# Kernel optimization log

Hardware: AMD Instinct MI355X
Metric: run time of the kernel (lower is better)

## Reference

```python
import jax, jax.numpy as jnp
import numpy as np

NUM_TRAIN = 256  # num_train_anchors
N, A, T = 8, 131072, 64


def _make_boxes(key, shape2):
    # shape2 = (..., 2) of (y, x); returns valid boxes (y1, x1, y2, x2) in [0, 1]
    k1, k2 = jax.random.split(key)
    c1 = jax.random.uniform(k1, shape2, dtype=jnp.float32)
    c2 = jax.random.uniform(k2, shape2, dtype=jnp.float32)
    lo = jnp.minimum(c1, c2)
    hi = jnp.maximum(c1, c2)
    return jnp.stack([lo[..., 0], lo[..., 1], hi[..., 0], hi[..., 1]], axis=-1)


def setup_inputs() -> dict:
    key = jax.random.key(0)
    ka, kt, kp, kn = jax.random.split(key, 4)
    return {
        "anchors": _make_boxes(ka, (N, A, 2)),
        "true_bboxes": _make_boxes(kt, (N, T, 2)),
        "rand_pos": jax.random.uniform(kp, (N, A), dtype=jnp.float32),
        "rand_neg": jax.random.uniform(kn, (N, A), dtype=jnp.float32),
    }


def _bbox_overlap(anchors, gt):
    # anchors [A,4], gt [T,4] -> IoU [A,T]
    ay1, ax1, ay2, ax2 = [anchors[:, i] for i in range(4)]
    gy1, gx1, gy2, gx2 = [gt[:, i] for i in range(4)]
    a_area = (ay2 - ay1) * (ax2 - ax1)                       # [A]
    g_area = (gy2 - gy1) * (gx2 - gx1)                       # [T]
    ih = jnp.clip(jnp.minimum(ay2[:, None], gy2[None, :]) - jnp.maximum(ay1[:, None], gy1[None, :]), 0.0)
    iw = jnp.clip(jnp.minimum(ax2[:, None], gx2[None, :]) - jnp.maximum(ax1[:, None], gx1[None, :]), 0.0)
    inter = ih * iw                                          # [A,T]
    union = a_area[:, None] + g_area[None, :] - inter
    return jnp.where(union > 0, inter / jnp.where(union > 0, union, 1.0), 0.0)


def _rank_of(scores):
    # rank[i] = position of element i in ascending sort of scores
    order = jnp.argsort(scores)
    return jnp.zeros(scores.shape[0], jnp.int32).at[order].set(jnp.arange(scores.shape[0], dtype=jnp.int32))


def _compute_bbox_deltas(anchors, gt):
    # standard (dy, dx, dh, dw) encoding with safe denominators
    ah = anchors[:, 2] - anchors[:, 0]
    aw = anchors[:, 3] - anchors[:, 1]
    acy = anchors[:, 0] + 0.5 * ah
    acx = anchors[:, 1] + 0.5 * aw
    gh = gt[:, 2] - gt[:, 0]
    gw = gt[:, 3] - gt[:, 1]
    gcy = gt[:, 0] + 0.5 * gh
    gcx = gt[:, 1] + 0.5 * gw
    ah_s = jnp.where(ah > 0, ah, 1.0)
    aw_s = jnp.where(aw > 0, aw, 1.0)
    gh_s = jnp.where(gh > 0, gh, 1.0)
    gw_s = jnp.where(gw > 0, gw, 1.0)
    return jnp.stack([(gcy - acy) / ah_s, (gcx - acx) / aw_s,
                      jnp.log(gh_s / ah_s), jnp.log(gw_s / aw_s)], axis=-1)


def _get_targets(anchors, gt, r_pos, r_neg):
    na = anchors.shape[0]
    # strip_out_of_bounds_anchors: zero out anchors falling outside [0,1]^2 (keeps static shape)
    inb = (anchors[:, 0] >= 0) & (anchors[:, 1] >= 0) & (anchors[:, 2] <= 1) & (anchors[:, 3] <= 1)
    anchors = jnp.where(inb[:, None], anchors, 0.0)

    overlaps = _bbox_overlap(anchors, gt)                    # [A,T]

    # --- class assignment ---
    iou_max_val = jnp.max(overlaps, axis=1)                  # [A]
    classes = jnp.full((na,), -1, jnp.int32)
    classes = jnp.where(iou_max_val < 0.3, 0, classes)
    iou_max_anchor = jnp.argmax(overlaps, axis=0)            # [T] best anchor per gt
    pos_anchor = jnp.zeros((na,), jnp.int32).at[iou_max_anchor].set(1)
    classes = jnp.where(pos_anchor > 0, 1, classes)
    classes = jnp.where(iou_max_val >= 0.7, 1, classes)

    # --- subsample positives to NUM_TRAIN//2 (uniform random subset) ---
    pos = classes > 0
    rank_p = _rank_of(jnp.where(pos, r_pos, jnp.inf))
    keep_pos = pos & (rank_p < NUM_TRAIN // 2)
    classes = jnp.where(pos & ~keep_pos, -1, classes)
    n_pos = jnp.sum(keep_pos.astype(jnp.int32))

    # --- subsample negatives to NUM_TRAIN - n_pos ---
    desired_neg = NUM_TRAIN - n_pos
    neg = classes == 0
    rank_n = _rank_of(jnp.where(neg, r_neg, jnp.inf))
    keep_neg = neg & (rank_n < desired_neg)
    classes = jnp.where(neg & ~keep_neg, -1, classes)

    # --- deltas for positive anchors ---
    best_gt = jnp.argmax(overlaps, axis=1)                   # [A]
    deltas = _compute_bbox_deltas(anchors, gt[best_gt])      # [A,4]
    deltas = jnp.where((classes > 0)[:, None], deltas, 0.0)
    return classes, deltas


def reference(anchors, true_bboxes, rand_pos, rand_neg):
    classes, deltas = jax.vmap(_get_targets)(anchors, true_bboxes, rand_pos, rand_neg)
    return classes, deltas
```

## Files before the change

kernel.cpp:

```cpp
#include <hip/hip_runtime.h>
#include <stdint.h>

#define N_B 8
#define A_N 131072
#define T_N 64
#define NUM_TRAIN 256
#define NEG_TAU 0.05f
#define ITEM_CAP 512
#define HSET 512
#define APT 2
#define SEG_A 512
#define GBLK_A 256
#define CAPP 128
#define BLK_C 128
#define SEG_C 1024

typedef unsigned long long u64;
typedef unsigned int u32;

__device__ __forceinline__ float iou_one(float ay1, float ax1, float ay2, float ax2,
                                         float a_area, float gy1, float gx1, float gy2,
                                         float gx2, float g_area) {
#pragma clang fp contract(off)
    float ih = fmaxf(fminf(ay2, gy2) - fmaxf(ay1, gy1), 0.0f);
    float iw = fmaxf(fminf(ax2, gx2) - fmaxf(ax1, gx1), 0.0f);
    float inter = ih * iw;
    float uni = (a_area + g_area) - inter;
    return uni > 0.0f ? inter / uni : 0.0f;
}

__global__ void __launch_bounds__(256) k_main(const float4* __restrict__ anchors4,
                                              const float4* __restrict__ gts4,
                                              const float* __restrict__ rpos,
                                              const float* __restrict__ rneg,
                                              unsigned char* __restrict__ preclass,
                                              long long* __restrict__ colpack,
                                              u64* __restrict__ pos_list,
                                              u64* __restrict__ neg_list,
                                              int* __restrict__ bcp, int* __restrict__ bcn) {
    __shared__ float4 gbox[T_N];
    __shared__ float gars[T_N];
    __shared__ u64 cmax[T_N];
    __shared__ int lcnt[2];
    int n = blockIdx.y, bx = blockIdx.x, tid = threadIdx.x, lane = tid & 63;
    int a0 = bx * SEG_A + tid;
    size_t nA = (size_t)n * A_N;

    if (tid < T_N) {
        float4 gb = gts4[n * T_N + tid];
        gbox[tid] = gb;
        {
#pragma clang fp contract(off)
            gars[tid] = (gb.z - gb.x) * (gb.w - gb.y);
        }
        cmax[tid] = 0;
    }
    if (tid < 2) lcnt[tid] = 0;
    __syncthreads();

    float ay1[APT], ax1[APT], ay2[APT], ax2[APT], aar[APT], vmax[APT];
#pragma unroll
    for (int k = 0; k < APT; k++) {
        float4 ab = anchors4[nA + a0 + k * 256];
        float y1 = ab.x, x1 = ab.y, y2 = ab.z, x2 = ab.w;
        bool inb = (y1 >= 0.f) && (x1 >= 0.f) && (y2 <= 1.f) && (x2 <= 1.f);
        if (!inb) { y1 = x1 = y2 = x2 = 0.f; }
        ay1[k] = y1; ax1[k] = x1; ay2[k] = y2; ax2[k] = x2;
        {
#pragma clang fp contract(off)
            aar[k] = (y2 - y1) * (x2 - x1);
        }
        vmax[k] = 0.f;
    }

#pragma unroll 4
    for (int jj = 0; jj < T_N; jj++) {
        int j = (lane + jj) & (T_N - 1);
        float4 gb = gbox[j];
        float gar = gars[j];
        float vb = iou_one(ay1[0], ax1[0], ay2[0], ax2[0], aar[0], gb.x, gb.y, gb.z, gb.w, gar);
        vmax[0] = fmaxf(vmax[0], vb);
        int kb = 0;
#pragma unroll
        for (int k = 1; k < APT; k++) {
            float v = iou_one(ay1[k], ax1[k], ay2[k], ax2[k], aar[k], gb.x, gb.y, gb.z, gb.w, gar);
            vmax[k] = fmaxf(vmax[k], v);
            if (v > vb) { vb = v; kb = k; }
        }
        u64 pk = ((u64)__float_as_uint(vb) << 32) | (u32)(~(u32)(a0 + (kb << 8)));
        atomicMax(&cmax[j], pk);
    }

    size_t segbase = ((size_t)(n * GBLK_A + bx)) << 7;
#pragma unroll
    for (int k = 0; k < APT; k++) {
        int a = a0 + k * 256;
        float vm = vmax[k];
        int c0 = (vm < 0.3f) ? 0 : ((vm >= 0.7f) ? 1 : -1);
        preclass[nA + a] = (unsigned char)(signed char)c0;
        if (c0 == 1) {
            int sl = atomicAdd(&lcnt[0], 1);
            if (sl < CAPP)
                pos_list[segbase + sl] = ((u64)__float_as_uint(rpos[nA + a]) << 32) | (u32)a;
        } else if (c0 == 0) {
            float r = rneg[nA + a];
            if (r < NEG_TAU) {
                int sl = atomicAdd(&lcnt[1], 1);
                if (sl < CAPP)
                    neg_list[segbase + sl] = ((u64)__float_as_uint(r) << 32) | (u32)a;
            }
        }
    }
    __syncthreads();
    if (tid < T_N) atomicMax(&colpack[(n << 6) + tid], (long long)cmax[tid]);
    if (tid == 0) {
        bcp[n * GBLK_A + bx] = lcnt[0] < CAPP ? lcnt[0] : CAPP;
        bcn[n * GBLK_A + bx] = lcnt[1] < CAPP ? lcnt[1] : CAPP;
    }
}

__device__ __forceinline__ bool in_hset(const int* hset, int a) {
    u32 h = ((u32)a * 2654435761u) >> 23 & (HSET - 1);
    while (true) {
        int v = hset[h];
        if (v == -1) return false;
        if (v == a) return true;
        h = (h + 1) & (HSET - 1);
    }
}

__device__ u64 select_kth2(const u64* lists, const int* scnt,
                           const u64* extras, int ecnt, const int* hset, bool use_excl,
                           int k, float scale, u64 ovf_all,
                           int* hist, u64* items, int* misc, int* wsum, u64* result) {
    int tid = threadIdx.x, lane = tid & 63, wid = tid >> 6;
    hist[tid] = 0;
    if (tid == 0) { misc[0] = 0; *result = ovf_all; }
    __syncthreads();

    int c = scnt[tid];
    const ulonglong2* b2 = (const ulonglong2*)(lists + ((size_t)tid << 7));
    int nch = (c + 1) >> 1;

    {
        ulonglong2 q;
        if (nch > 0) q = b2[0];
        for (int ci = 0; ci < nch; ci++) {
            ulonglong2 qn;
            if (ci + 1 < nch) qn = b2[ci + 1];
            {
                u64 p = q.x; int a = (int)(u32)p;
                if (!use_excl || !in_hset(hset, a)) {
                    float v = __uint_as_float((u32)(p >> 32));
                    int bb = (int)(v * scale); bb = bb > 255 ? 255 : bb;
                    atomicAdd(&hist[bb], 1);
                }
            }
            if (2 * ci + 1 < c) {
                u64 p = q.y; int a = (int)(u32)p;
                if (!use_excl || !in_hset(hset, a)) {
                    float v = __uint_as_float((u32)(p >> 32));
                    int bb = (int)(v * scale); bb = bb > 255 ? 255 : bb;
                    atomicAdd(&hist[bb], 1);
                }
            }
            q = qn;
        }
    }
    for (int i = tid; i < ecnt; i += 256) {
        float v = __uint_as_float((u32)(extras[i] >> 32));
        int bb = (int)(v * scale); bb = bb > 255 ? 255 : bb;
        atomicAdd(&hist[bb], 1);
    }
    __syncthreads();

    int h = hist[tid], v = h;
#pragma unroll
    for (int d = 1; d < 64; d <<= 1) {
        int t = __shfl_up(v, d, 64);
        if (lane >= d) v += t;
    }
    if (lane == 63) wsum[wid] = v;
    __syncthreads();
    int base = 0;
    for (int w = 0; w < wid; w++) base += wsum[w];
    int total = wsum[0] + wsum[1] + wsum[2] + wsum[3];
    int incl = base + v, exc = incl - h;
    if (k >= exc && k < incl) { misc[1] = tid; misc[2] = exc; }
    __syncthreads();
    if (k >= total) return ovf_all;
    int b = misc[1], before = misc[2];

    {
        ulonglong2 q;
        if (nch > 0) q = b2[0];
        for (int ci = 0; ci < nch; ci++) {
            ulonglong2 qn;
            if (ci + 1 < nch) qn = b2[ci + 1];
            {
                u64 p = q.x; int a = (int)(u32)p;
                if (!use_excl || !in_hset(hset, a)) {
                    float vv = __uint_as_float((u32)(p >> 32));
                    int bn = (int)(vv * scale); bn = bn > 255 ? 255 : bn;
                    if (bn == b) { int ix = atomicAdd(&misc[0], 1); if (ix < ITEM_CAP) items[ix] = p; }
                }
            }
            if (2 * ci + 1 < c) {
                u64 p = q.y; int a = (int)(u32)p;
                if (!use_excl || !in_hset(hset, a)) {
                    float vv = __uint_as_float((u32)(p >> 32));
                    int bn = (int)(vv * scale); bn = bn > 255 ? 255 : bn;
                    if (bn == b) { int ix = atomicAdd(&misc[0], 1); if (ix < ITEM_CAP) items[ix] = p; }
                }
            }
            q = qn;
        }
    }
    for (int i = tid; i < ecnt; i += 256) {
        u64 p = extras[i];
        float vv = __uint_as_float((u32)(p >> 32));
        int bn = (int)(vv * scale); bn = bn > 255 ? 255 : bn;
        if (bn == b) { int ix = atomicAdd(&misc[0], 1); if (ix < ITEM_CAP) items[ix] = p; }
    }
    __syncthreads();
    int m = misc[0]; m = m < ITEM_CAP ? m : ITEM_CAP;
    int target = k - before;
    for (int i = tid; i < m; i += 256) {
        u64 p = items[i];
        int r = 0;
        for (int j = 0; j < m; j++) r += (items[j] < p);
        if (r == target) *result = p;
    }
    __syncthreads();
    u64 res = *result;
    __syncthreads();
    return res;
}

__global__ void __launch_bounds__(256) k_B(const u64* __restrict__ pos_list,
                                           const u64* __restrict__ neg_list,
                                           const int* __restrict__ bcp,
                                           const int* __restrict__ bcn,
                                           const long long* __restrict__ colpack,
                                           const unsigned char* __restrict__ preclass,
                                           const float* __restrict__ rpos,
                                           int* __restrict__ wnr_g,
                                           u64* __restrict__ cutoff) {
    __shared__ int sbp[GBLK_A], sbn[GBLK_A];
    __shared__ int wnrs[T_N];
    __shared__ u64 extras[T_N];
    __shared__ int hist[256];
    __shared__ u64 items[ITEM_CAP];
    __shared__ int hset[HSET];
    __shared__ int misc[4];
    __shared__ int wsum[4];
    __shared__ int shr[10];
    __shared__ u64 result;
    int n = blockIdx.y, role = blockIdx.x, tid = threadIdx.x, lane = tid & 63, wid = tid >> 6;
    size_t nA = (size_t)n * A_N;

    int pv = bcp[n * GBLK_A + tid];
    sbp[tid] = pv;
    sbn[tid] = bcn[n * GBLK_A + tid];
#pragma unroll
    for (int off = 32; off > 0; off >>= 1) pv += __shfl_xor(pv, off, 64);
    if (lane == 0) shr[wid] = pv;

    for (int i = tid; i < HSET; i += 256) hset[i] = -1;
    __syncthreads();

    if (tid < T_N) {
        u64 m = (u64)colpack[(n << 6) + tid];
        int w = (int)(~(u32)(m & 0xFFFFFFFFull));
        wnrs[tid] = w;
        if (role == 0) wnr_g[n * T_N + tid] = w;
        u32 hh = ((u32)w * 2654435761u) >> 23 & (HSET - 1);
        while (true) {
            int old = atomicCAS(&hset[hh], -1, w);
            if (old == -1 || old == w) break;
            hh = (hh + 1) & (HSET - 1);
        }
    }
    __syncthreads();
    if (tid < T_N) {
        int w = wnrs[tid];
        bool dup = false;
        for (int t2 = 0; t2 < tid; t2++) dup |= (wnrs[t2] == w);
        int pc = (int)(signed char)preclass[nA + w];
        bool val = !dup && (pc != 1);
        u64 mask = __ballot(val);
        if (role == 0 && val) {
            int ix = (int)__popcll(mask & ((1ull << lane) - 1));
            extras[ix] = ((u64)__float_as_uint(rpos[nA + w]) << 32) | (u32)w;
        }
        if (tid == 0) shr[8] = (int)__popcll(mask);
    }
    __syncthreads();
    int extra_cnt = shr[8];
    int P = shr[0] + shr[1] + shr[2] + shr[3] + extra_cnt;

    if (role == 0) {
        u64 cpos = ~0ull;
        if (NUM_TRAIN / 2 < P)
            cpos = select_kth2(pos_list + (((size_t)n * GBLK_A) << 7), sbp,
                               extras, extra_cnt, hset, false,
                               NUM_TRAIN / 2, 256.0f, ~0ull,
                               hist, items, misc, wsum, &result);
        if (tid == 0) cutoff[2 * n] = cpos;
    } else {
        int n_pos = P < NUM_TRAIN / 2 ? P : NUM_TRAIN / 2;
        int k_neg = NUM_TRAIN - n_pos;
        u64 cneg = select_kth2(neg_list + (((size_t)n * GBLK_A) << 7), sbn,
                               nullptr, 0, hset, true,
                               k_neg, 256.0f / NEG_TAU, ((u64)__float_as_uint(NEG_TAU) << 32),
                               hist, items, misc, wsum, &result);
        if (tid == 0) cutoff[2 * n + 1] = cneg;
    }
}

__global__ void __launch_bounds__(256) k_C(const float4* __restrict__ anchors4,
                                           const float4* __restrict__ gts4,
                                           const u32* __restrict__ preclass32,
                                           const int* __restrict__ wnr_g,
                                           const float4* __restrict__ rpos4,
                                           const float4* __restrict__ rneg4,
                                           const u64* __restrict__ cutoff,
                                           float4* __restrict__ out_classes4,
                                           float4* __restrict__ out_deltas) {
    __shared__ float4 gbox[T_N];
    __shared__ float gars[T_N];
    __shared__ u32 wbm[32];
    int n = blockIdx.y, bx = blockIdx.x, tid = threadIdx.x;
    size_t nA = (size_t)n * A_N;
    if (tid < 32) wbm[tid] = 0;
    __syncthreads();
    if (tid < T_N) {
        float4 gb = gts4[n * T_N + tid];
        gbox[tid] = gb;
        {
#pragma clang fp contract(off)
            gars[tid] = (gb.z - gb.x) * (gb.w - gb.y);
        }
        int w = wnr_g[n * T_N + tid];
        int d = w - bx * SEG_C;
        if ((u32)d < (u32)SEG_C) atomicOr(&wbm[d >> 5], 1u << (d & 31));
    }
    __syncthreads();

    size_t gi4 = nA / 4 + bx * 256 + tid;
    u32 pcw = preclass32[gi4];
    float4 rp = rpos4[gi4];
    float4 rn = rneg4[gi4];
    float rpv[4] = {rp.x, rp.y, rp.z, rp.w};
    float rnv[4] = {rn.x, rn.y, rn.z, rn.w};
    int a0 = (bx * 256 + tid) * 4;
    u64 cp = cutoff[2 * n], cn = cutoff[2 * n + 1];

    u32 marked = (wbm[tid >> 3] >> ((tid & 7) * 4)) & 0xF;

    float fcv[4];
#pragma unroll
    for (int j = 0; j < 4; j++) {
        int c = (int)(signed char)((pcw >> (8 * j)) & 0xFF);
        if ((marked >> j) & 1) c = 1;
        int a = a0 + j;
        int fc = -1;
        if (c == 1) {
            u64 p = ((u64)__float_as_uint(rpv[j]) << 32) | (u32)a;
            fc = (p < cp) ? 1 : -1;
        } else if (c == 0) {
            u64 p = ((u64)__float_as_uint(rnv[j]) << 32) | (u32)a;
            fc = (p < cn) ? 0 : -1;
        }
        fcv[j] = (float)fc;

        float4 d = make_float4(0.f, 0.f, 0.f, 0.f);
        if (fc == 1) {
            float4 ab = anchors4[nA + a];
            float ay1 = ab.x, ax1 = ab.y, ay2 = ab.z, ax2 = ab.w;
            bool inb = (ay1 >= 0.f) && (ax1 >= 0.f) && (ay2 <= 1.f) && (ax2 <= 1.f);
            if (!inb) { ay1 = ax1 = ay2 = ax2 = 0.f; }
            float a_area;
            {
#pragma clang fp contract(off)
                a_area = (ay2 - ay1) * (ax2 - ax1);
            }
            float vm = 0.f; int jb = 0;
            for (int t = 0; t < T_N; t++) {
                float4 gb = gbox[t];
                float v = iou_one(ay1, ax1, ay2, ax2, a_area, gb.x, gb.y, gb.z, gb.w, gars[t]);
                bool g = v > vm;
                vm = g ? v : vm;
                jb = g ? t : jb;
            }
            float4 gb = gbox[jb];
            float ah = ay2 - ay1, aw = ax2 - ax1;
            float acy = ay1 + 0.5f * ah, acx = ax1 + 0.5f * aw;
            float gh = gb.z - gb.x, gw = gb.w - gb.y;
            float gcy = gb.x + 0.5f * gh, gcx = gb.y + 0.5f * gw;
            float ah_s = ah > 0.f ? ah : 1.f, aw_s = aw > 0.f ? aw : 1.f;
            float gh_s = gh > 0.f ? gh : 1.f, gw_s = gw > 0.f ? gw : 1.f;
            d.x = (gcy - acy) / ah_s;
            d.y = (gcx - acx) / aw_s;
            d.z = logf(gh_s / ah_s);
            d.w = logf(gw_s / aw_s);
        }
        out_deltas[nA + a] = d;
    }
    out_classes4[gi4] = make_float4(fcv[0], fcv[1], fcv[2], fcv[3]);
}

extern "C" void kernel_launch(void* const* d_in, const int* in_sizes, int n_in,
                              void* d_out, int out_size, void* d_ws, size_t ws_size,
                              hipStream_t stream) {
    const float4* anchors4 = (const float4*)d_in[0];
    const float4* gts4     = (const float4*)d_in[1];
    const float*  rpos     = (const float*)d_in[2];
    const float*  rneg     = (const float*)d_in[3];

    char* p = (char*)d_ws;
    u64* cutoff   = (u64*)p;  p += 2 * N_B * sizeof(u64);
    long long* colpack = (long long*)p; p += N_B * T_N * sizeof(long long);
    u64* pos_list = (u64*)p;  p += (size_t)N_B * GBLK_A * CAPP * sizeof(u64);
    u64* neg_list = (u64*)p;  p += (size_t)N_B * GBLK_A * CAPP * sizeof(u64);
    unsigned char* preclass = (unsigned char*)p; p += (size_t)N_B * A_N;
    int* bcp  = (int*)p;  p += N_B * GBLK_A * sizeof(int);
    int* bcn  = (int*)p;  p += N_B * GBLK_A * sizeof(int);
    int* wnr  = (int*)p;  p += N_B * T_N * sizeof(int);

    float4* out_classes4 = (float4*)d_out;
    float4* out_deltas   = (float4*)((float*)d_out + (size_t)N_B * A_N);

    k_main<<<dim3(GBLK_A, N_B), 256, 0, stream>>>(anchors4, gts4, rpos, rneg, preclass,
                                                  colpack, pos_list, neg_list, bcp, bcn);
    k_B<<<dim3(2, N_B), 256, 0, stream>>>(pos_list, neg_list, bcp, bcn, colpack,
                                          preclass, rpos, wnr, cutoff);
    k_C<<<dim3(BLK_C, N_B), 256, 0, stream>>>(anchors4, gts4, (const u32*)preclass, wnr,
                                              (const float4*)rpos, (const float4*)rneg,
                                              cutoff, out_classes4, out_deltas);
}
```

Before: 175.2 us.

## Fuse selection kernel into main pass via last-block-done pattern

Folds the per-image cutoff selection (formerly a separate 2-block-per-image kernel) into the tail of the main IoU kernel: each block bumps a per-image counter and the last finishing block runs both positive and negative k-th selection serially. This removes one kernel launch and its dependency gap, and also simplifies the per-GT argmax packing for two anchors per thread. In exchange it adds a memset launch, inflates static shared memory of the main kernel (possibly lowering occupancy), and serializes the two selections that were previously done in parallel blocks.

```diff
diff --git a/kernel.cpp b/kernel.cpp
--- a/kernel.cpp
+++ b/kernel.cpp
@@ -29,6 +29,124 @@
     return uni > 0.0f ? inter / uni : 0.0f;
 }
 
+__device__ __forceinline__ bool in_hset(const int* hset, int a) {
+    u32 h = ((u32)a * 2654435761u) >> 23 & (HSET - 1);
+    while (true) {
+        int v = hset[h];
+        if (v == -1) return false;
+        if (v == a) return true;
+        h = (h + 1) & (HSET - 1);
+    }
+}
+
+__device__ u64 select_kth2(const u64* lists, const int* scnt,
+                           const u64* extras, int ecnt, const int* hset, bool use_excl,
+                           int k, float scale, u64 ovf_all,
+                           int* hist, u64* items, int* misc, int* wsum, u64* result) {
+    int tid = threadIdx.x, lane = tid & 63, wid = tid >> 6;
+    hist[tid] = 0;
+    if (tid == 0) { misc[0] = 0; *result = ovf_all; }
+    __syncthreads();
+
+    int c = scnt[tid];
+    const ulonglong2* b2 = (const ulonglong2*)(lists + ((size_t)tid << 7));
+    int nch = (c + 1) >> 1;
+
+    {
+        ulonglong2 q;
+        if (nch > 0) q = b2[0];
+        for (int ci = 0; ci < nch; ci++) {
+            ulonglong2 qn;
+            if (ci + 1 < nch) qn = b2[ci + 1];
+            {
+                u64 p = q.x; int a = (int)(u32)p;
+                if (!use_excl || !in_hset(hset, a)) {
+                    float v = __uint_as_float((u32)(p >> 32));
+                    int bb = (int)(v * scale); bb = bb > 255 ? 255 : bb;
+                    atomicAdd(&hist[bb], 1);
+                }
+            }
+            if (2 * ci + 1 < c) {
+                u64 p = q.y; int a = (int)(u32)p;
+                if (!use_excl || !in_hset(hset, a)) {
+                    float v = __uint_as_float((u32)(p >> 32));
+                    int bb = (int)(v * scale); bb = bb > 255 ? 255 : bb;
+                    atomicAdd(&hist[bb], 1);
+                }
+            }
+            q = qn;
+        }
+    }
+    for (int i = tid; i < ecnt; i += 256) {
+        float v = __uint_as_float((u32)(extras[i] >> 32));
+        int bb = (int)(v * scale); bb = bb > 255 ? 255 : bb;
+        atomicAdd(&hist[bb], 1);
+    }
+    __syncthreads();
+
+    int h = hist[tid], v = h;
+#pragma unroll
+    for (int d = 1; d < 64; d <<= 1) {
+        int t = __shfl_up(v, d, 64);
+        if (lane >= d) v += t;
+    }
+    if (lane == 63) wsum[wid] = v;
+    __syncthreads();
+    int base = 0;
+    for (int w = 0; w < wid; w++) base += wsum[w];
+    int total = wsum[0] + wsum[1] + wsum[2] + wsum[3];
+    int incl = base + v, exc = incl - h;
+    if (k >= exc && k < incl) { misc[1] = tid; misc[2] = exc; }
+    __syncthreads();
+    if (k >= total) return ovf_all;
+    int b = misc[1], before = misc[2];
+
+    {
+        ulonglong2 q;
+        if (nch > 0) q = b2[0];
+        for (int ci = 0; ci < nch; ci++) {
+            ulonglong2 qn;
+            if (ci + 1 < nch) qn = b2[ci + 1];
+            {
+                u64 p = q.x; int a = (int)(u32)p;
+                if (!use_excl || !in_hset(hset, a)) {
+                    float vv = __uint_as_float((u32)(p >> 32));
+                    int bn = (int)(vv * scale); bn = bn > 255 ? 255 : bn;
+                    if (bn == b) { int ix = atomicAdd(&misc[0], 1); if (ix < ITEM_CAP) items[ix] = p; }
+                }
+            }
+            if (2 * ci + 1 < c) {
+                u64 p = q.y; int a = (int)(u32)p;
+                if (!use_excl || !in_hset(hset, a)) {
+                    float vv = __uint_as_float((u32)(p >> 32));
+                    int bn = (int)(vv * scale); bn = bn > 255 ? 255 : bn;
+                    if (bn == b) { int ix = atomicAdd(&misc[0], 1); if (ix < ITEM_CAP) items[ix] = p; }
+                }
+            }
+            q = qn;
+        }
+    }
+    for (int i = tid; i < ecnt; i += 256) {
+        u64 p = extras[i];
+        float vv = __uint_as_float((u32)(p >> 32));
+        int bn = (int)(vv * scale); bn = bn > 255 ? 255 : bn;
+        if (bn == b) { int ix = atomicAdd(&misc[0], 1); if (ix < ITEM_CAP) items[ix] = p; }
+    }
+    __syncthreads();
+    int m = misc[0]; m = m < ITEM_CAP ? m : ITEM_CAP;
+    int target = k - before;
+    for (int i = tid; i < m; i += 256) {
+        u64 p = items[i];
+        int r = 0;
+        for (int j = 0; j < m; j++) r += (items[j] < p);
+        if (r == target) *result = p;
+    }
+    __syncthreads();
+    u64 res = *result;
+    __syncthreads();
+    return res;
+}
+
 __global__ void __launch_bounds__(256) k_main(const float4* __restrict__ anchors4,
                                               const float4* __restrict__ gts4,
                                               const float* __restrict__ rpos,
@@ -37,11 +155,26 @@
                                               long long* __restrict__ colpack,
                                               u64* __restrict__ pos_list,
                                               u64* __restrict__ neg_list,
-                                              int* __restrict__ bcp, int* __restrict__ bcn) {
+                                              int* __restrict__ bcp, int* __restrict__ bcn,
+                                              int* __restrict__ done,
+                                              int* __restrict__ wnr_g,
+                                              u64* __restrict__ cutoff) {
     __shared__ float4 gbox[T_N];
     __shared__ float gars[T_N];
     __shared__ u64 cmax[T_N];
     __shared__ int lcnt[2];
+    __shared__ int isLast;
+    __shared__ int sbp[GBLK_A], sbn[GBLK_A];
+    __shared__ int wnrs[T_N];
+    __shared__ u64 extras[T_N];
+    __shared__ int hist[256];
+    __shared__ u64 items[ITEM_CAP];
+    __shared__ int hset[HSET];
+    __shared__ int misc[4];
+    __shared__ int wsum[4];
+    __shared__ int shr[10];
+    __shared__ u64 result;
+
     int n = blockIdx.y, bx = blockIdx.x, tid = threadIdx.x, lane = tid & 63;
     int a0 = bx * SEG_A + tid;
     size_t nA = (size_t)n * A_N;
@@ -72,22 +205,20 @@
         }
         vmax[k] = 0.f;
     }
+    u32 na0 = ~(u32)a0, na1 = ~(u32)(a0 + 256);
 
 #pragma unroll 4
     for (int jj = 0; jj < T_N; jj++) {
         int j = (lane + jj) & (T_N - 1);
         float4 gb = gbox[j];
         float gar = gars[j];
-        float vb = iou_one(ay1[0], ax1[0], ay2[0], ax2[0], aar[0], gb.x, gb.y, gb.z, gb.w, gar);
-        vmax[0] = fmaxf(vmax[0], vb);
-        int kb = 0;
-#pragma unroll
-        for (int k = 1; k < APT; k++) {
-            float v = iou_one(ay1[k], ax1[k], ay2[k], ax2[k], aar[k], gb.x, gb.y, gb.z, gb.w, gar);
-            vmax[k] = fmaxf(vmax[k], v);
-            if (v > vb) { vb = v; kb = k; }
-        }
-        u64 pk = ((u64)__float_as_uint(vb) << 32) | (u32)(~(u32)(a0 + (kb << 8)));
+        float v0 = iou_one(ay1[0], ax1[0], ay2[0], ax2[0], aar[0], gb.x, gb.y, gb.z, gb.w, gar);
+        float v1 = iou_one(ay1[1], ax1[1], ay2[1], ax2[1], aar[1], gb.x, gb.y, gb.z, gb.w, gar);
+        vmax[0] = fmaxf(vmax[0], v0);
+        vmax[1] = fmaxf(vmax[1], v1);
+        float vb = v1 > v0 ? v1 : v0;
+        u32 nsel = v1 > v0 ? na1 : na0;
+        u64 pk = ((u64)__float_as_uint(vb) << 32) | nsel;
         atomicMax(&cmax[j], pk);
     }
 
@@ -117,148 +248,14 @@
         bcp[n * GBLK_A + bx] = lcnt[0] < CAPP ? lcnt[0] : CAPP;
         bcn[n * GBLK_A + bx] = lcnt[1] < CAPP ? lcnt[1] : CAPP;
     }
-}
-
-__device__ __forceinline__ bool in_hset(const int* hset, int a) {
-    u32 h = ((u32)a * 2654435761u) >> 23 & (HSET - 1);
-    while (true) {
-        int v = hset[h];
-        if (v == -1) return false;
-        if (v == a) return true;
-        h = (h + 1) & (HSET - 1);
-    }
-}
-
-__device__ u64 select_kth2(const u64* lists, const int* scnt,
-                           const u64* extras, int ecnt, const int* hset, bool use_excl,
-                           int k, float scale, u64 ovf_all,
-                           int* hist, u64* items, int* misc, int* wsum, u64* result) {
-    int tid = threadIdx.x, lane = tid & 63, wid = tid >> 6;
-    hist[tid] = 0;
-    if (tid == 0) { misc[0] = 0; *result = ovf_all; }
-    __syncthreads();
-
-    int c = scnt[tid];
-    const ulonglong2* b2 = (const ulonglong2*)(lists + ((size_t)tid << 7));
-    int nch = (c + 1) >> 1;
-
-    {
-        ulonglong2 q;
-        if (nch > 0) q = b2[0];
-        for (int ci = 0; ci < nch; ci++) {
-            ulonglong2 qn;
-            if (ci + 1 < nch) qn = b2[ci + 1];
-            {
-                u64 p = q.x; int a = (int)(u32)p;
-                if (!use_excl || !in_hset(hset, a)) {
-                    float v = __uint_as_float((u32)(p >> 32));
-                    int bb = (int)(v * scale); bb = bb > 255 ? 255 : bb;
-                    atomicAdd(&hist[bb], 1);
-                }
-            }
-            if (2 * ci + 1 < c) {
-                u64 p = q.y; int a = (int)(u32)p;
-                if (!use_excl || !in_hset(hset, a)) {
-                    float v = __uint_as_float((u32)(p >> 32));
-                    int bb = (int)(v * scale); bb = bb > 255 ? 255 : bb;
-                    atomicAdd(&hist[bb], 1);
-                }
-            }
-            q = qn;
-        }
-    }
-    for (int i = tid; i < ecnt; i += 256) {
-        float v = __uint_as_float((u32)(extras[i] >> 32));
-        int bb = (int)(v * scale); bb = bb > 255 ? 255 : bb;
-        atomicAdd(&hist[bb], 1);
-    }
-    __syncthreads();
-
-    int h = hist[tid], v = h;
-#pragma unroll
-    for (int d = 1; d < 64; d <<= 1) {
-        int t = __shfl_up(v, d, 64);
-        if (lane >= d) v += t;
-    }
-    if (lane == 63) wsum[wid] = v;
-    __syncthreads();
-    int base = 0;
-    for (int w = 0; w < wid; w++) base += wsum[w];
-    int total = wsum[0] + wsum[1] + wsum[2] + wsum[3];
-    int incl = base + v, exc = incl - h;
-    if (k >= exc && k < incl) { misc[1] = tid; misc[2] = exc; }
-    __syncthreads();
-    if (k >= total) return ovf_all;
-    int b = misc[1], before = misc[2];
-
-    {
-        ulonglong2 q;
-        if (nch > 0) q = b2[0];
-        for (int ci = 0; ci < nch; ci++) {
-            ulonglong2 qn;
-            if (ci + 1 < nch) qn = b2[ci + 1];
-            {
-                u64 p = q.x; int a = (int)(u32)p;
-                if (!use_excl || !in_hset(hset, a)) {
-                    float vv = __uint_as_float((u32)(p >> 32));
-                    int bn = (int)(vv * scale); bn = bn > 255 ? 255 : bn;
-                    if (bn == b) { int ix = atomicAdd(&misc[0], 1); if (ix < ITEM_CAP) items[ix] = p; }
-                }
-            }
-            if (2 * ci + 1 < c) {
-                u64 p = q.y; int a = (int)(u32)p;
-                if (!use_excl || !in_hset(hset, a)) {
-                    float vv = __uint_as_float((u32)(p >> 32));
-                    int bn = (int)(vv * scale); bn = bn > 255 ? 255 : bn;
-                    if (bn == b) { int ix = atomicAdd(&misc[0], 1); if (ix < ITEM_CAP) items[ix] = p; }
-                }
-            }
-            q = qn;
-        }
-    }
-    for (int i = tid; i < ecnt; i += 256) {
-        u64 p = extras[i];
-        float vv = __uint_as_float((u32)(p >> 32));
-        int bn = (int)(vv * scale); bn = bn > 255 ? 255 : bn;
-        if (bn == b) { int ix = atomicAdd(&misc[0], 1); if (ix < ITEM_CAP) items[ix] = p; }
-    }
-    __syncthreads();
-    int m = misc[0]; m = m < ITEM_CAP ? m : ITEM_CAP;
-    int target = k - before;
-    for (int i = tid; i < m; i += 256) {
-        u64 p = items[i];
-        int r = 0;
-        for (int j = 0; j < m; j++) r += (items[j] < p);
-        if (r == target) *result = p;
-    }
-    __syncthreads();
-    u64 res = *result;
-    __syncthreads();
-    return res;
-}
-
-__global__ void __launch_bounds__(256) k_B(const u64* __restrict__ pos_list,
-                                           const u64* __restrict__ neg_list,
-                                           const int* __restrict__ bcp,
-                                           const int* __restrict__ bcn,
-                                           const long long* __restrict__ colpack,
-                                           const unsigned char* __restrict__ preclass,
-                                           const float* __restrict__ rpos,
-                                           int* __restrict__ wnr_g,
-                                           u64* __restrict__ cutoff) {
-    __shared__ int sbp[GBLK_A], sbn[GBLK_A];
-    __shared__ int wnrs[T_N];
-    __shared__ u64 extras[T_N];
-    __shared__ int hist[256];
-    __shared__ u64 items[ITEM_CAP];
-    __shared__ int hset[HSET];
-    __shared__ int misc[4];
-    __shared__ int wsum[4];
-    __shared__ int shr[10];
-    __shared__ u64 result;
-    int n = blockIdx.y, role = blockIdx.x, tid = threadIdx.x, lane = tid & 63, wid = tid >> 6;
-    size_t nA = (size_t)n * A_N;
-
+
+    __threadfence();
+    if (tid == 0) isLast = (atomicAdd(&done[n], 1) == GBLK_A - 1);
+    __syncthreads();
+    if (!isLast) return;
+    __threadfence();
+
+    int wid = tid >> 6;
     int pv = bcp[n * GBLK_A + tid];
     sbp[tid] = pv;
     sbn[tid] = bcn[n * GBLK_A + tid];
@@ -273,7 +270,7 @@
         u64 m = (u64)colpack[(n << 6) + tid];
         int w = (int)(~(u32)(m & 0xFFFFFFFFull));
         wnrs[tid] = w;
-        if (role == 0) wnr_g[n * T_N + tid] = w;
+        wnr_g[n * T_N + tid] = w;
         u32 hh = ((u32)w * 2654435761u) >> 23 & (HSET - 1);
         while (true) {
             int old = atomicCAS(&hset[hh], -1, w);
@@ -289,7 +286,7 @@
         int pc = (int)(signed char)preclass[nA + w];
         bool val = !dup && (pc != 1);
         u64 mask = __ballot(val);
-        if (role == 0 && val) {
+        if (val) {
             int ix = (int)__popcll(mask & ((1ull << lane) - 1));
             extras[ix] = ((u64)__float_as_uint(rpos[nA + w]) << 32) | (u32)w;
         }
@@ -299,23 +296,19 @@
     int extra_cnt = shr[8];
     int P = shr[0] + shr[1] + shr[2] + shr[3] + extra_cnt;
 
-    if (role == 0) {
-        u64 cpos = ~0ull;
-        if (NUM_TRAIN / 2 < P)
-            cpos = select_kth2(pos_list + (((size_t)n * GBLK_A) << 7), sbp,
-                               extras, extra_cnt, hset, false,
-                               NUM_TRAIN / 2, 256.0f, ~0ull,
-                               hist, items, misc, wsum, &result);
-        if (tid == 0) cutoff[2 * n] = cpos;
-    } else {
-        int n_pos = P < NUM_TRAIN / 2 ? P : NUM_TRAIN / 2;
-        int k_neg = NUM_TRAIN - n_pos;
-        u64 cneg = select_kth2(neg_list + (((size_t)n * GBLK_A) << 7), sbn,
-                               nullptr, 0, hset, true,
-                               k_neg, 256.0f / NEG_TAU, ((u64)__float_as_uint(NEG_TAU) << 32),
-                               hist, items, misc, wsum, &result);
-        if (tid == 0) cutoff[2 * n + 1] = cneg;
-    }
+    u64 cpos = ~0ull;
+    if (NUM_TRAIN / 2 < P)
+        cpos = select_kth2(pos_list + (((size_t)n * GBLK_A) << 7), sbp,
+                           extras, extra_cnt, hset, false,
+                           NUM_TRAIN / 2, 256.0f, ~0ull,
+                           hist, items, misc, wsum, &result);
+    int n_pos = P < NUM_TRAIN / 2 ? P : NUM_TRAIN / 2;
+    int k_neg = NUM_TRAIN - n_pos;
+    u64 cneg = select_kth2(neg_list + (((size_t)n * GBLK_A) << 7), sbn,
+                           nullptr, 0, hset, true,
+                           k_neg, 256.0f / NEG_TAU, ((u64)__float_as_uint(NEG_TAU) << 32),
+                           hist, items, misc, wsum, &result);
+    if (tid == 0) { cutoff[2 * n] = cpos; cutoff[2 * n + 1] = cneg; }
 }
 
 __global__ void __launch_bounds__(256) k_C(const float4* __restrict__ anchors4,
@@ -427,14 +420,15 @@
     int* bcp  = (int*)p;  p += N_B * GBLK_A * sizeof(int);
     int* bcn  = (int*)p;  p += N_B * GBLK_A * sizeof(int);
     int* wnr  = (int*)p;  p += N_B * T_N * sizeof(int);
+    int* done = (int*)p;  p += N_B * sizeof(int);
 
     float4* out_classes4 = (float4*)d_out;
     float4* out_deltas   = (float4*)((float*)d_out + (size_t)N_B * A_N);
 
+    hipMemsetAsync(done, 0, N_B * sizeof(int), stream);
     k_main<<<dim3(GBLK_A, N_B), 256, 0, stream>>>(anchors4, gts4, rpos, rneg, preclass,
-                                                  colpack, pos_list, neg_list, bcp, bcn);
-    k_B<<<dim3(2, N_B), 256, 0, stream>>>(pos_list, neg_list, bcp, bcn, colpack,
-                                          preclass, rpos, wnr, cutoff);
+                                                  colpack, pos_list, neg_list, bcp, bcn,
+                                                  done, wnr, cutoff);
     k_C<<<dim3(BLK_C, N_B), 256, 0, stream>>>(anchors4, gts4, (const u32*)preclass, wnr,
                                               (const float4*)rpos, (const float4*)rneg,
                                               cutoff, out_classes4, out_deltas);
```

Result: slower. 354.5 us (+102.4%).
